# Optimization experiments

Measured on AMD Instinct MI355X. Metric: run time of the kernel, lower is better.

## Reference

```python
import jax, jax.numpy as jnp
import numpy as np

DIM = 96
NH = 8
HID = int(DIM * 2.66)  # 255
B, H, W = 2, 128, 128


def _conv(x, w, groups=1, pad=0):
    # NCHW conv, stride 1
    return jax.lax.conv_general_dilated(
        x, w, (1, 1), ((pad, pad), (pad, pad)),
        feature_group_count=groups,
        dimension_numbers=('NCHW', 'OIHW', 'NCHW'))


def _ln(x, w, b):
    # WithBias LayerNorm over the channel axis (torch does to_3d -> LN(dim) -> to_4d)
    mu = x.mean(axis=1, keepdims=True)
    var = ((x - mu) ** 2).mean(axis=1, keepdims=True)
    return (x - mu) * jax.lax.rsqrt(var + 1e-5) * w[None, :, None, None] + b[None, :, None, None]


def setup_inputs() -> dict:
    key = jax.random.key(0)
    ks = jax.random.split(key, 16)
    d, h2, h4 = DIM, 2 * HID, 4 * HID
    def n(k, shape, s):
        return jax.random.normal(k, shape, jnp.float32) * s
    return {
        'x': jax.random.normal(ks[0], (B, d, H, W), jnp.float32),
        'norm1_w': jnp.ones((d,), jnp.float32), 'norm1_b': jnp.zeros((d,), jnp.float32),
        'qkv_w': n(ks[1], (3 * d, d, 1, 1), 0.05),
        'qkv_dw_w': n(ks[2], (3 * d, 1, 3, 3), 0.1),
        'proj_w': n(ks[3], (d, d, 1, 1), 0.05),
        'temperature': jnp.ones((NH, 1, 1), jnp.float32),
        'thresholdweight': 0.2 * jnp.ones((4, 1, 1, 1), jnp.float32),
        'attn_w1': n(ks[4], (4, NH, NH), 0.2), 'attn_b1': jnp.zeros((4, NH), jnp.float32),
        'attn_w2': n(ks[5], (4, NH, NH), 0.2), 'attn_b2': jnp.zeros((4, NH), jnp.float32),
        'norm2_w': jnp.ones((d,), jnp.float32), 'norm2_b': jnp.zeros((d,), jnp.float32),
        'in_w': n(ks[6], (h2, d, 1, 1), 0.05),
        'main_w': n(ks[7], (h4, 1, 3, 3), 0.1),   # groups=2*HID, 2 out per group
        'lp_w': n(ks[8], (h4, 1, 3, 3), 0.1),     # depthwise
        'hp_w': n(ks[9], (h4, 1, 3, 3), 0.1),     # depthwise
        'ld_w': n(ks[10], (HID, 4, 3, 3), 0.1),   # groups=HID, 4 in per group
        'hd_w': n(ks[11], (HID, 4, 3, 3), 0.1),
        'out_w': n(ks[12], (d, h2, 1, 1), 0.05),
    }


def reference(x, norm1_w, norm1_b, qkv_w, qkv_dw_w, proj_w, temperature,
              thresholdweight, attn_w1, attn_b1, attn_w2, attn_b2,
              norm2_w, norm2_b, in_w, main_w, lp_w, hp_w, ld_w, hd_w, out_w):
    b, c, hh, ww = x.shape
    ch = c // NH
    # ---- STS channel attention ----
    xn = _ln(x, norm1_w, norm1_b)
    qkv = _conv(_conv(xn, qkv_w), qkv_dw_w, groups=3 * c, pad=1)
    q, k, v = jnp.split(qkv, 3, axis=1)
    q = q.reshape(b, NH, ch, hh * ww)
    k = k.reshape(b, NH, ch, hh * ww)
    v = v.reshape(b, NH, ch, hh * ww)
    q = q / jnp.maximum(jnp.linalg.norm(q, axis=-1, keepdims=True), 1e-12)
    k = k / jnp.maximum(jnp.linalg.norm(k, axis=-1, keepdims=True), 1e-12)
    attn = jnp.einsum('bhcn,bhdn->bhcd', q, k) * temperature[None]  # [b,NH,ch,ch]

    def sts_gen(w1, b1, w2, b2):
        a_abs = jnp.abs(attn)
        avg = a_abs.mean(axis=(-2, -1))                       # [b, NH] (GAP)
        g = jax.nn.sigmoid(jnp.maximum(avg @ w1.T + b1, 0.0) @ w2.T + b2)
        thr = (avg * g)[:, :, None, None]
        return jnp.sign(attn) * jnp.maximum(a_abs - thr, 0.0)

    comp = jax.vmap(sts_gen)(attn_w1, attn_b1, attn_w2, attn_b2)  # [4,b,NH,ch,ch]
    comp = jax.nn.softmax(comp, axis=-1)
    attn_c = jnp.sum(comp * thresholdweight.reshape(4, 1, 1, 1, 1), axis=0)
    out = jnp.einsum('bhcd,bhdn->bhcn', attn_c, v).reshape(b, c, hh, ww)
    x = x + _conv(out, proj_w)

    # ---- DeCoupleConvv3 FFN ----
    y = _ln(x, norm2_w, norm2_b)
    y = _conv(y, in_w)                                         # [b, 2*HID, h, w]
    y = jax.nn.relu(_conv(y, main_w, groups=2 * HID, pad=1))   # [b, 4*HID, h, w]
    avg_w = jnp.full((4 * HID, 1, 3, 3), 1.0 / 9.0, y.dtype)   # fixed, non-trainable
    yp = jnp.pad(y, ((0, 0), (0, 0), (1, 1), (1, 1)), mode='edge')  # replicate pad
    l = _conv(yp, avg_w, groups=4 * HID, pad=0)
    hb = y - l
    l = jax.nn.relu(_conv(l, lp_w, groups=4 * HID, pad=1))
    hb = jax.nn.relu(_conv(hb, hp_w, groups=4 * HID, pad=1))
    l_tol, l_toh = jnp.split(l, [2 * HID], axis=1)
    h_toh, h_tol = jnp.split(hb, [2 * HID], axis=1)
    l2 = jax.nn.relu(_conv(jnp.concatenate([l_tol, h_tol], axis=1), ld_w, groups=HID, pad=1))
    h2 = jax.nn.relu(_conv(jnp.concatenate([h_toh, l_toh], axis=1), hd_w, groups=HID, pad=1))
    ffo = _conv(jnp.concatenate([l2, h2], axis=1), out_w)
    return x + ffo
```

## Files before the change

kernel.cpp:

```cpp
#include <hip/hip_runtime.h>
#include <hip/hip_bf16.h>
#include <hip/hip_fp16.h>

#define NB   2
#define NC   96
#define NW   128
#define NPIX 16384
#define NHD  8
#define CHD  12
#define HIDC 255
#define H2C  510
#define H4C  1020

typedef __hip_bfloat16 bf16;
typedef unsigned short u16;
typedef unsigned int   u32;
typedef __half2 h2t;

typedef __attribute__((ext_vector_type(8))) __bf16 bfrag;
typedef __attribute__((ext_vector_type(4))) float  ffrag;

__device__ __forceinline__ float bfu(u16 u)  { return __uint_as_float(((u32)u) << 16); }
__device__ __forceinline__ float bflo(u32 u) { return __uint_as_float(u << 16); }
__device__ __forceinline__ float bfhi(u32 u) { return __uint_as_float(u & 0xffff0000u); }
__device__ __forceinline__ u16 f2u16(float a) {
    bf16 x = __float2bfloat16(a); return *(u16*)&x;
}
__device__ __forceinline__ u32 packbf(float a, float b) {
    return (u32)f2u16(a) | ((u32)f2u16(b) << 16);
}
__device__ __forceinline__ uint4 pack8(const float o[8]) {
    uint4 r; r.x = packbf(o[0], o[1]); r.y = packbf(o[2], o[3]);
    r.z = packbf(o[4], o[5]); r.w = packbf(o[6], o[7]); return r;
}

__device__ __forceinline__ h2t H2u(u32 v) { return __builtin_bit_cast(h2t, v); }
__device__ __forceinline__ u32 U32h(h2t v) { return __builtin_bit_cast(u32, v); }
__device__ __forceinline__ h2t relu2(h2t v) {
    u32 r, u = U32h(v);
    asm("v_pk_max_f16 %0, %1, 0" : "=v"(r) : "v"(u));
    return H2u(r);
}
__device__ __forceinline__ h2t wtap(const h2t* a, int idx) {
    u32 u = U32h(a[idx >> 1]);
    u32 r = (idx & 1) ? ((u & 0xFFFF0000u) | (u >> 16)) : ((u << 16) | (u & 0xFFFFu));
    return H2u(r);
}

struct Trip { h2t L, C, R; };
__device__ __forceinline__ Trip shift3(h2t c2, bool repl, int lane) {
    u32 d = U32h(c2);
    u32 up = (u32)__shfl_up((int)d, 1);
    u32 dn = (u32)__shfl_down((int)d, 1);
    if (lane == 0)  up = repl ? (d << 16) : 0u;
    if (lane == 63) dn = repl ? (d >> 16) : 0u;
    Trip t; t.C = c2;
    t.L = H2u((up >> 16) | (d << 16));
    t.R = H2u((d >> 16) | (dn << 16));
    return t;
}
__device__ __forceinline__ h2t ldrow2(const u16* base, int row, int lane) {
    return ((unsigned)row < 128u) ? *(const h2t*)(base + row * NW + lane * 2) : H2u(0u);
}
#define CONV3(W, c, T, Pa, Pb, Pc)                                             \
    Pc = __hfma2(wtap(W, (c)*9+0), T.L, __hfma2(wtap(W, (c)*9+1), T.C,         \
         __hfma2(wtap(W, (c)*9+2), T.R, Pc)));                                 \
    Pb = __hfma2(wtap(W, (c)*9+3), T.L, __hfma2(wtap(W, (c)*9+4), T.C,         \
         __hfma2(wtap(W, (c)*9+5), T.R, Pb)));                                 \
    Pa = __hfma2(wtap(W, (c)*9+6), T.L, __hfma2(wtap(W, (c)*9+7), T.C,         \
         __hfma2(wtap(W, (c)*9+8), T.R, Pa)));

__global__ __launch_bounds__(64) void ffnstream_kernel(
    const u16* __restrict__ yi, const float* __restrict__ main_w,
    const float* __restrict__ lp_w, const float* __restrict__ hp_w,
    const float* __restrict__ ld_w, const float* __restrict__ hd_w,
    u16* __restrict__ cat) {
    const int lane = threadIdx.x;
    const int g = blockIdx.y;
    const int R0 = blockIdx.x * 32, R1 = R0 + 32;
    const int L0 = max(R0 - 2, 0), L1 = min(R1 + 1, 127);
    const int P0 = max(R0 - 1, 0), P1 = min(R1, 127);
    const u16* yib = yi + (size_t)blockIdx.z * H2C * NPIX;
    u16* catb = cat + (size_t)blockIdx.z * H2C * NPIX;
    const u16* s0p = yib + (size_t)(2 * g) * NPIX;
    const u16* s1p = yib + (size_t)(2 * g + 1) * NPIX;

    h2t wm[18], wl[18], wh[18], wd[18], we[18];
    {
        const float* pm = main_w + 36 * g;
        const float* pl = lp_w + 36 * g;
        const float* ph = hp_w + 36 * g;
        const float* pd = ld_w + 36 * g;
        const float* pe = hd_w + 36 * g;
        #pragma unroll
        for (int k = 0; k < 18; ++k) {
            wm[k] = __halves2half2(__float2half(pm[2*k]), __float2half(pm[2*k+1]));
            wl[k] = __halves2half2(__float2half(pl[2*k]), __float2half(pl[2*k+1]));
            wh[k] = __halves2half2(__float2half(ph[2*k]), __float2half(ph[2*k+1]));
            wd[k] = __halves2half2(__float2half(pd[2*k]), __float2half(pd[2*k+1]));
            we[k] = __halves2half2(__float2half(pe[2*k]), __float2half(pe[2*k+1]));
        }
    }
    const h2t z = H2u(0u);
    const __half k9h = __float2half(1.f / 9.f);
    const h2t k9 = __halves2half2(k9h, k9h);

    h2t ymP0[4], ymP1[4], ymP2[4];
    h2t ymRa[4], ymRb[4], ymRc[4];
    h2t lpP0[4], lpP1[4], lpP2[4];
    h2t hpP0[4], hpP1[4], hpP2[4];
    h2t cd0 = z, cd1 = z, cd2 = z;
    h2t ce0 = z, ce1 = z, ce2 = z;
    #pragma unroll
    for (int c = 0; c < 4; ++c) {
        ymP0[c] = ymP1[c] = ymP2[c] = z;
        ymRa[c] = ymRb[c] = ymRc[c] = z;
        lpP0[c] = lpP1[c] = lpP2[c] = z;
        hpP0[c] = hpP1[c] = hpP2[c] = z;
    }

    const int ys = max(R0 - 3, 0) - 1;
    const int ye = R1 + 3;
    h2t cur0 = ldrow2(s0p, ys, lane),     cur1 = ldrow2(s1p, ys, lane);
    h2t nx10 = ldrow2(s0p, ys + 1, lane), nx11 = ldrow2(s1p, ys + 1, lane);
    #pragma unroll 3
    for (int yy = ys; yy <= ye; ++yy) {
        h2t nx20 = ldrow2(s0p, yy + 2, lane), nx21 = ldrow2(s1p, yy + 2, lane);
        {
            Trip t0 = shift3(cur0, false, lane);
            Trip t1 = shift3(cur1, false, lane);
            CONV3(wm, 0, t0, ymP0[0], ymP1[0], ymP2[0]);
            CONV3(wm, 1, t0, ymP0[1], ymP1[1], ymP2[1]);
            CONV3(wm, 2, t1, ymP0[2], ymP1[2], ymP2[2]);
            CONV3(wm, 3, t1, ymP0[3], ymP1[3], ymP2[3]);
        }
        #pragma unroll
        for (int c = 0; c < 4; ++c) {
            h2t n = relu2(ymP0[c]);
            ymRc[c] = ymRb[c]; ymRb[c] = ymRa[c]; ymRa[c] = n;
            ymP0[c] = ymP1[c]; ymP1[c] = ymP2[c]; ymP2[c] = z;
        }
        int y_l = yy - 2;
        if (y_l >= L0 && y_l <= L1) {
            #pragma unroll
            for (int c = 0; c < 4; ++c) {
                h2t top = (y_l == 0)   ? ymRb[c] : ymRc[c];
                h2t bot = (y_l == 127) ? ymRb[c] : ymRa[c];
                h2t vs = __hadd2(__hadd2(top, ymRb[c]), bot);
                Trip tv = shift3(vs, true, lane);
                h2t l  = __hmul2(__hadd2(__hadd2(tv.L, tv.C), tv.R), k9);
                h2t hb = __hsub2(ymRb[c], l);
                Trip tl = shift3(l, false, lane);
                CONV3(wl, c, tl, lpP0[c], lpP1[c], lpP2[c]);
                Trip th = shift3(hb, false, lane);
                CONV3(wh, c, th, hpP0[c], hpP1[c], hpP2[c]);
            }
        }
        int y_p = yy - 3;
        {
            h2t lpN[4], hpN[4];
            #pragma unroll
            for (int c = 0; c < 4; ++c) {
                lpN[c] = relu2(lpP0[c]); hpN[c] = relu2(hpP0[c]);
                lpP0[c] = lpP1[c]; lpP1[c] = lpP2[c]; lpP2[c] = z;
                hpP0[c] = hpP1[c]; hpP1[c] = hpP2[c]; hpP2[c] = z;
            }
            if (y_p >= P0 && y_p <= P1) {
                #pragma unroll
                for (int c = 0; c < 4; ++c) {
                    bool low = (4 * g + c) < H2C;
                    h2t sld = low ? lpN[c] : hpN[c];
                    h2t shd = low ? hpN[c] : lpN[c];
                    Trip ts = shift3(sld, false, lane);
                    CONV3(wd, c, ts, cd0, cd1, cd2);
                    Trip tu = shift3(shd, false, lane);
                    CONV3(we, c, tu, ce0, ce1, ce2);
                }
            }
        }
        int y_c = yy - 4;
        if (y_c >= R0 && y_c < R1) {
            float a0 = fmaxf(__low2float(cd0), 0.f), a1 = fmaxf(__high2float(cd0), 0.f);
            float b0 = fmaxf(__low2float(ce0), 0.f), b1 = fmaxf(__high2float(ce0), 0.f);
            *(u32*)(catb + (size_t)g * NPIX + y_c * NW + lane * 2) = packbf(a0, a1);
            *(u32*)(catb + (size_t)(HIDC + g) * NPIX + y_c * NW + lane * 2) = packbf(b0, b1);
        }
        cd0 = cd1; cd1 = cd2; cd2 = z;
        ce0 = ce1; ce1 = ce2; ce2 = z;
        cur0 = nx10; cur1 = nx11;
        nx10 = nx20; nx11 = nx21;
    }
}

template <typename TOut, bool RES, int OFMT>
__global__ __launch_bounds__(256) void gemm1x1_kernel(
    const u16* __restrict__ Bm, const float* __restrict__ Am,
    const float* __restrict__ res, TOut* __restrict__ Cm,
    int M, int K, size_t strideB, size_t strideC, size_t strideA) {
    __shared__ u16 Ash[64 * 40];
    __shared__ u16 Bsh[128 * 40];
    const u16* Bz = Bm + (size_t)blockIdx.z * strideB;
    const float* Az = Am + (size_t)blockIdx.z * strideA;
    int n0 = blockIdx.x * 128;
    int m0 = blockIdx.y * 64;
    int tid = threadIdx.x;
    int w = tid >> 6, l15 = tid & 15, q = (tid & 63) >> 4;
    int amm = tid >> 2, akc = (tid & 3) * 8;
    int bkk = tid >> 3, bs0 = tid & 7;

    ffrag acc[8];
    #pragma unroll
    for (int nt = 0; nt < 8; ++nt)
        #pragma unroll
        for (int e = 0; e < 4; ++e) acc[nt][e] = 0.f;

    for (int k0 = 0; k0 < K; k0 += 32) {
        {
            int gm = m0 + amm;
            float f[8];
            #pragma unroll
            for (int e = 0; e < 8; ++e) {
                int gk = k0 + akc + e;
                f[e] = (gm < M && gk < K) ? Az[(size_t)gm * K + gk] : 0.f;
            }
            u32* dst = (u32*)&Ash[amm * 40 + akc];
            #pragma unroll
            for (int e = 0; e < 4; ++e) dst[e] = packbf(f[2 * e], f[2 * e + 1]);
        }
        {
            int gk = k0 + bkk;
            bool ok = gk < K;
            const u16* src = Bz + (size_t)gk * NPIX + n0;
            #pragma unroll
            for (int pass = 0; pass < 2; ++pass) {
                int nn = (bs0 + pass * 8) * 8;
                if (ok) {
                    uint4 v = *(const uint4*)(src + nn);
                    Bsh[(nn + 0) * 40 + bkk] = (u16)(v.x & 0xffff);
                    Bsh[(nn + 1) * 40 + bkk] = (u16)(v.x >> 16);
                    Bsh[(nn + 2) * 40 + bkk] = (u16)(v.y & 0xffff);
                    Bsh[(nn + 3) * 40 + bkk] = (u16)(v.y >> 16);
                    Bsh[(nn + 4) * 40 + bkk] = (u16)(v.z & 0xffff);
                    Bsh[(nn + 5) * 40 + bkk] = (u16)(v.z >> 16);
                    Bsh[(nn + 6) * 40 + bkk] = (u16)(v.w & 0xffff);
                    Bsh[(nn + 7) * 40 + bkk] = (u16)(v.w >> 16);
                } else {
                    #pragma unroll
                    for (int e = 0; e < 8; ++e) Bsh[(nn + e) * 40 + bkk] = 0;
                }
            }
        }
        __syncthreads();
        bfrag af = *(const bfrag*)&Ash[(w * 16 + l15) * 40 + q * 8];
        #pragma unroll
        for (int nt = 0; nt < 8; ++nt) {
            bfrag bf = *(const bfrag*)&Bsh[(nt * 16 + l15) * 40 + q * 8];
            acc[nt] = __builtin_amdgcn_mfma_f32_16x16x32_bf16(af, bf, acc[nt], 0, 0, 0);
        }
        __syncthreads();
    }
    TOut* Cz = Cm + (size_t)blockIdx.z * strideC;
    const float* rz = res + (RES ? (size_t)blockIdx.z * strideC : 0);
    int mrow = m0 + w * 16 + q * 4;
    #pragma unroll
    for (int nt = 0; nt < 8; ++nt) {
        int col = n0 + nt * 16 + l15;
        #pragma unroll
        for (int r = 0; r < 4; ++r) {
            int row = mrow + r;
            if (row < M) {
                float v = acc[nt][r];
                if (RES) v += rz[(size_t)row * NPIX + col];
                if constexpr (OFMT == 0) {
                    ((float*)Cz)[(size_t)row * NPIX + col] = v;
                } else if constexpr (OFMT == 1) {
                    ((u16*)Cz)[(size_t)row * NPIX + col] = f2u16(v);
                } else {
                    __half hh = __float2half(v);
                    ((u16*)Cz)[(size_t)row * NPIX + col] = __builtin_bit_cast(u16, hh);
                }
            }
        }
    }
}

__global__ __launch_bounds__(256) void ln_kernel(
    const float* __restrict__ x, const float* __restrict__ g,
    const float* __restrict__ bta, u16* __restrict__ out) {
    int blk = blockIdx.x;
    int b = blk >> 9;
    int p = ((blk & 511) << 5) + (threadIdx.x & 31);
    int cg = threadIdx.x >> 5;
    const float* xb = x + (size_t)b * NC * NPIX + p;
    float v[12]; float s = 0.f, s2 = 0.f;
    #pragma unroll
    for (int j = 0; j < 12; ++j) {
        float t = xb[(size_t)(cg * 12 + j) * NPIX];
        v[j] = t; s += t; s2 += t * t;
    }
    __shared__ float ss[8][32], qq[8][32], smu[32], sinv[32];
    ss[cg][threadIdx.x & 31] = s; qq[cg][threadIdx.x & 31] = s2;
    __syncthreads();
    if (threadIdx.x < 32) {
        float S = 0.f, Q = 0.f;
        #pragma unroll
        for (int k = 0; k < 8; ++k) { S += ss[k][threadIdx.x]; Q += qq[k][threadIdx.x]; }
        float mu = S * (1.f / NC);
        float var = Q * (1.f / NC) - mu * mu;
        smu[threadIdx.x] = mu; sinv[threadIdx.x] = rsqrtf(var + 1e-5f);
    }
    __syncthreads();
    float mu = smu[threadIdx.x & 31], inv = sinv[threadIdx.x & 31];
    u16* ob = out + (size_t)b * NC * NPIX + p;
    #pragma unroll
    for (int j = 0; j < 12; ++j) {
        int c = cg * 12 + j;
        ob[(size_t)c * NPIX] = f2u16((v[j] - mu) * inv * g[c] + bta[c]);
    }
}

__device__ __forceinline__ void load_row_zpad(const u16* ib, int iy, int x0, float a[10]) {
    if (iy < 0 || iy >= NW) {
        #pragma unroll
        for (int k = 0; k < 10; ++k) a[k] = 0.f;
        return;
    }
    const u16* rp = ib + iy * NW;
    uint4 v = *(const uint4*)(rp + x0);
    a[1]=bflo(v.x); a[2]=bfhi(v.x); a[3]=bflo(v.y); a[4]=bfhi(v.y);
    a[5]=bflo(v.z); a[6]=bfhi(v.z); a[7]=bflo(v.w); a[8]=bfhi(v.w);
    a[0] = (x0 > 0)   ? bfu(rp[x0 - 1]) : 0.f;
    a[9] = (x0 < 120) ? bfu(rp[x0 + 8]) : 0.f;
}

template <bool RELU>
__global__ __launch_bounds__(256) void dwconv3x3_kernel(
    const u16* __restrict__ in, const float* __restrict__ w,
    u16* __restrict__ out, int CHN, int ICN, int idiv) {
    int id = blockIdx.x * 256 + threadIdx.x;
    int ty = id >> 4, tx = id & 15;
    int y0 = ty * 4, x0 = tx * 8;
    int b = blockIdx.y / CHN, oc = blockIdx.y % CHN;
    int ic = oc / idiv;
    const u16* ib = in + ((size_t)b * ICN + ic) * NPIX;
    float a[6][10];
    #pragma unroll
    for (int k = 0; k < 6; ++k) load_row_zpad(ib, y0 - 1 + k, x0, a[k]);
    const float* wr = w + (size_t)oc * 9;
    float w9[9];
    #pragma unroll
    for (int k = 0; k < 9; ++k) w9[k] = wr[k];
    u16* ob = out + ((size_t)b * CHN + oc) * NPIX + y0 * NW + x0;
    #pragma unroll
    for (int jr = 0; jr < 4; ++jr) {
        float o[8];
        #pragma unroll
        for (int j = 0; j < 8; ++j) {
            float s = 0.f;
            #pragma unroll
            for (int r = 0; r < 3; ++r)
                #pragma unroll
                for (int kx = 0; kx < 3; ++kx)
                    s += w9[r * 3 + kx] * a[jr + r][j + kx];
            o[j] = RELU ? fmaxf(s, 0.f) : s;
        }
        *(uint4*)(ob + jr * NW) = pack8(o);
    }
}

__global__ __launch_bounds__(256) void qknorm_kernel(
    const u16* __restrict__ qkv2, float* __restrict__ scales) {
    int r = blockIdx.x;
    int b = r / 192, ch = r % 192;
    const u16* src = qkv2 + ((size_t)b * 288 + ch) * NPIX;
    float s = 0.f;
    for (int p = threadIdx.x * 8; p < NPIX; p += 2048) {
        uint4 v = *(const uint4*)(src + p);
        float f[8];
        f[0]=bflo(v.x); f[1]=bfhi(v.x); f[2]=bflo(v.y); f[3]=bfhi(v.y);
        f[4]=bflo(v.z); f[5]=bfhi(v.z); f[6]=bflo(v.w); f[7]=bfhi(v.w);
        #pragma unroll
        for (int k = 0; k < 8; ++k) s += f[k] * f[k];
    }
    #pragma unroll
    for (int off = 32; off > 0; off >>= 1) s += __shfl_down(s, off, 64);
    __shared__ float part[4];
    int wid = threadIdx.x >> 6;
    if ((threadIdx.x & 63) == 0) part[wid] = s;
    __syncthreads();
    if (threadIdx.x == 0) {
        float tot = part[0] + part[1] + part[2] + part[3];
        scales[r] = 1.f / fmaxf(sqrtf(tot), 1e-12f);
    }
}

__global__ __launch_bounds__(256) void attn_kernel(
    const u16* __restrict__ qkv2, float* __restrict__ attn_raw) {
    int blk = blockIdx.y;
    int slice = blockIdx.x;
    int i = blk % CHD; int h = (blk / CHD) % NHD; int b = blk / (CHD * NHD);
    const u16* q = qkv2 + ((size_t)b * 288 + h * CHD + i) * NPIX;
    const u16* k = qkv2 + ((size_t)b * 288 + 96 + h * CHD) * NPIX;
    float acc[CHD];
    #pragma unroll
    for (int j = 0; j < CHD; ++j) acc[j] = 0.f;
    int p0 = slice * 4096;
    #pragma unroll
    for (int it = 0; it < 2; ++it) {
        int p = p0 + it * 2048 + threadIdx.x * 8;
        uint4 qv = *(const uint4*)(q + p);
        float qf[8];
        qf[0]=bflo(qv.x); qf[1]=bfhi(qv.x); qf[2]=bflo(qv.y); qf[3]=bfhi(qv.y);
        qf[4]=bflo(qv.z); qf[5]=bfhi(qv.z); qf[6]=bflo(qv.w); qf[7]=bfhi(qv.w);
        #pragma unroll
        for (int j = 0; j < CHD; ++j) {
            uint4 kv = *(const uint4*)(k + (size_t)j * NPIX + p);
            float s = qf[0]*bflo(kv.x) + qf[1]*bfhi(kv.x) + qf[2]*bflo(kv.y) + qf[3]*bfhi(kv.y)
                    + qf[4]*bflo(kv.z) + qf[5]*bfhi(kv.z) + qf[6]*bflo(kv.w) + qf[7]*bfhi(kv.w);
            acc[j] += s;
        }
    }
    __shared__ float part[4][CHD];
    int wid = threadIdx.x >> 6, lane = threadIdx.x & 63;
    #pragma unroll
    for (int j = 0; j < CHD; ++j) {
        float v = acc[j];
        #pragma unroll
        for (int off = 32; off > 0; off >>= 1) v += __shfl_down(v, off, 64);
        if (lane == 0) part[wid][j] = v;
    }
    __syncthreads();
    if (threadIdx.x < CHD) {
        int j = threadIdx.x;
        float d = part[0][j] + part[1][j] + part[2][j] + part[3][j];
        atomicAdd(&attn_raw[(size_t)blk * CHD + j], d);
    }
}

__global__ __launch_bounds__(256) void sts_kernel(
    const float* __restrict__ attn, const float* __restrict__ scl,
    const float* __restrict__ temp, const float* __restrict__ tw,
    const float* __restrict__ w1, const float* __restrict__ b1,
    const float* __restrict__ w2, const float* __restrict__ b2,
    const float* __restrict__ proj_w, float* __restrict__ Wm) {
    int b = blockIdx.x;
    __shared__ float sat[NHD * CHD * CHD];
    __shared__ float sac[NHD * CHD * CHD];
    __shared__ float avg[NHD];
    __shared__ float thr[4][NHD];
    for (int idx = threadIdx.x; idx < NHD * CHD * CHD; idx += 256) {
        int h = idx / (CHD * CHD); int r = idx % (CHD * CHD);
        int i = r / CHD, j = r % CHD;
        sat[idx] = attn[(size_t)b * NHD * CHD * CHD + idx]
                 * scl[b * 192 + h * CHD + i] * scl[b * 192 + 96 + h * CHD + j] * temp[h];
    }
    __syncthreads();
    if (threadIdx.x < NHD) {
        float s = 0.f;
        for (int t = 0; t < CHD * CHD; ++t) s += fabsf(sat[threadIdx.x * CHD * CHD + t]);
        avg[threadIdx.x] = s * (1.f / (CHD * CHD));
    }
    __syncthreads();
    if (threadIdx.x < 4) {
        int s = threadIdx.x;
        float t1[NHD];
        for (int hp = 0; hp < NHD; ++hp) {
            float u = b1[s * NHD + hp];
            for (int h = 0; h < NHD; ++h) u += avg[h] * w1[s * 64 + hp * NHD + h];
            t1[hp] = fmaxf(u, 0.f);
        }
        for (int hp = 0; hp < NHD; ++hp) {
            float u = b2[s * NHD + hp];
            for (int h = 0; h < NHD; ++h) u += t1[h] * w2[s * 64 + hp * NHD + h];
            float gg = 1.f / (1.f + expf(-u));
            thr[s][hp] = avg[hp] * gg;
        }
    }
    __syncthreads();
    if (threadIdx.x < NHD * CHD) {
        int h = threadIdx.x / CHD, i = threadIdx.x % CHD;
        const float* arow = sat + (h * CHD + i) * CHD;
        float acc[CHD];
        #pragma unroll
        for (int j = 0; j < CHD; ++j) acc[j] = 0.f;
        for (int s = 0; s < 4; ++s) {
            float comp[CHD]; float m = -1e30f;
            #pragma unroll
            for (int j = 0; j < CHD; ++j) {
                float a = arow[j];
                float sg = (a > 0.f) ? 1.f : ((a < 0.f) ? -1.f : 0.f);
                float c = sg * fmaxf(fabsf(a) - thr[s][h], 0.f);
                comp[j] = c; m = fmaxf(m, c);
            }
            float sum = 0.f;
            #pragma unroll
            for (int j = 0; j < CHD; ++j) { comp[j] = expf(comp[j] - m); sum += comp[j]; }
            float wts2v = tw[s] / sum;
            #pragma unroll
            for (int j = 0; j < CHD; ++j) acc[j] += wts2v * comp[j];
        }
        for (int j = 0; j < CHD; ++j)
            sac[(h * CHD + i) * CHD + j] = acc[j];
    }
    __syncthreads();
    float* Wb = Wm + (size_t)b * NC * NC;
    for (int idx = threadIdx.x; idx < NC * NC; idx += 256) {
        int m = idx / NC, col = idx % NC;
        int h = col / CHD, j = col % CHD;
        const float* pr = proj_w + m * NC + h * CHD;
        const float* ar = sac + h * CHD * CHD + j;
        float s = 0.f;
        #pragma unroll
        for (int i = 0; i < CHD; ++i) s += pr[i] * ar[i * CHD];
        Wb[idx] = s;
    }
}

extern "C" void kernel_launch(void* const* d_in, const int* in_sizes, int n_in,
                              void* d_out, int out_size, void* d_ws, size_t ws_size,
                              hipStream_t stream) {
    const float* x       = (const float*)d_in[0];
    const float* norm1_w = (const float*)d_in[1];
    const float* norm1_b = (const float*)d_in[2];
    const float* qkv_w   = (const float*)d_in[3];
    const float* qkv_dw  = (const float*)d_in[4];
    const float* proj_w  = (const float*)d_in[5];
    const float* temp    = (const float*)d_in[6];
    const float* thw     = (const float*)d_in[7];
    const float* aw1     = (const float*)d_in[8];
    const float* ab1     = (const float*)d_in[9];
    const float* aw2     = (const float*)d_in[10];
    const float* ab2     = (const float*)d_in[11];
    const float* norm2_w = (const float*)d_in[12];
    const float* norm2_b = (const float*)d_in[13];
    const float* in_w    = (const float*)d_in[14];
    const float* main_w  = (const float*)d_in[15];
    const float* lp_w    = (const float*)d_in[16];
    const float* hp_w    = (const float*)d_in[17];
    const float* ld_w    = (const float*)d_in[18];
    const float* hd_w    = (const float*)d_in[19];
    const float* out_w   = (const float*)d_in[20];
    float* out = (float*)d_out;

    char* ws = (char*)d_ws;
    float* x1    = (float*)(ws + 0);
    u16*   xnb   = (u16*)(ws + 12582912);
    u16*   qkv1  = (u16*)(ws + 18874368);
    u16*   qkv2  = (u16*)(ws + 37748736);
    float* scl   = (float*)(ws + 56623104);
    float* attn  = (float*)(ws + 56639488);
    char*  F0    = ws + 56672256;
    float* Wm    = (float*)(ws + 56655872);
    const size_t S_full = 33423360;
    bool full = ws_size >= (size_t)56672256 + S_full;

    dim3 blk(256);
    ln_kernel<<<dim3(NB * NPIX / 32), blk, 0, stream>>>(x, norm1_w, norm1_b, xnb);
    gemm1x1_kernel<u16, false, 1><<<dim3(128, 5, NB), blk, 0, stream>>>(
        xnb, qkv_w, nullptr, qkv1, 288, 96, (size_t)NC * NPIX, (size_t)288 * NPIX, 0);
    dwconv3x3_kernel<false><<<dim3(2, NB * 288), blk, 0, stream>>>(
        qkv1, qkv_dw, qkv2, 288, 288, 1);
    qknorm_kernel<<<dim3(NB * 192), blk, 0, stream>>>(qkv2, scl);
    (void)hipMemsetAsync(attn, 0, (size_t)NB * NHD * CHD * CHD * sizeof(float), stream);
    attn_kernel<<<dim3(4, NB * NHD * CHD), blk, 0, stream>>>(qkv2, attn);
    sts_kernel<<<dim3(NB), blk, 0, stream>>>(attn, scl, temp, thw, aw1, ab1, aw2, ab2,
                                             proj_w, Wm);
    gemm1x1_kernel<float, true, 0><<<dim3(128, 2, NB), blk, 0, stream>>>(
        qkv2 + (size_t)192 * NPIX, Wm, x, x1, 96, 96,
        (size_t)288 * NPIX, (size_t)NC * NPIX, (size_t)NC * NC);
    ln_kernel<<<dim3(NB * NPIX / 32), blk, 0, stream>>>(x1, norm2_w, norm2_b, xnb);
    if (full) {
        u16* yi  = qkv1;
        u16* cat = (u16*)F0;
        gemm1x1_kernel<u16, false, 2><<<dim3(128, 8, NB), blk, 0, stream>>>(
            xnb, in_w, nullptr, yi, H2C, 96, (size_t)NC * NPIX, (size_t)H2C * NPIX, 0);
        ffnstream_kernel<<<dim3(4, HIDC, NB), dim3(64), 0, stream>>>(
            yi, main_w, lp_w, hp_w, ld_w, hd_w, cat);
        gemm1x1_kernel<float, true, 0><<<dim3(128, 2, NB), blk, 0, stream>>>(
            cat, out_w, x1, out, 96, H2C, (size_t)H2C * NPIX, (size_t)NC * NPIX, 0);
    } else {
        for (int b = 0; b < NB; ++b) {
            u16* yi  = qkv1;
            u16* cat = qkv2;
            gemm1x1_kernel<u16, false, 2><<<dim3(128, 8, 1), blk, 0, stream>>>(
                xnb + (size_t)b * NC * NPIX, in_w, nullptr, yi, H2C, 96, 0, 0, 0);
            ffnstream_kernel<<<dim3(4, HIDC, 1), dim3(64), 0, stream>>>(
                yi, main_w, lp_w, hp_w, ld_w, hd_w, cat);
            gemm1x1_kernel<float, true, 0><<<dim3(128, 2, 1), blk, 0, stream>>>(
                cat, out_w, x1 + (size_t)b * NC * NPIX, out + (size_t)b * NC * NPIX,
                96, H2C, 0, 0, 0);
        }
    }
}
```

Measured before the change: 361.1 us.

## Fuse LayerNorm into 1x1 GEMMs and q/k norm into depthwise conv

Removes both standalone LayerNorm kernels. The qkv and FFN-input 1x1 GEMMs now compute per-pixel mean and variance from the fp32 input and normalize while staging the B tile, so the bf16 normalized intermediate is no longer written and read back. The q/k L2-norm pass is folded into the depthwise conv, which accumulates squared sums by atomicAdd into a zero-initialized buffer, and the sts kernel now takes the reciprocal sqrt and splits its abs-sum reduction. The cost is that every m-block of a GEMM recomputes the LN statistics and reads fp32 input instead of bf16, and the atomics make the reduction order non-deterministic.

```diff
diff --git a/kernel.cpp b/kernel.cpp
--- a/kernel.cpp
+++ b/kernel.cpp
@@ -192,15 +192,20 @@
     }
 }
 
-template <typename TOut, bool RES, int OFMT>
+template <typename TOut, bool RES, int OFMT, bool LNF = false>
 __global__ __launch_bounds__(256) void gemm1x1_kernel(
     const u16* __restrict__ Bm, const float* __restrict__ Am,
     const float* __restrict__ res, TOut* __restrict__ Cm,
-    int M, int K, size_t strideB, size_t strideC, size_t strideA) {
+    int M, int K, size_t strideB, size_t strideC, size_t strideA,
+    const float* __restrict__ xf, const float* __restrict__ lng,
+    const float* __restrict__ lnb) {
     __shared__ u16 Ash[64 * 40];
     __shared__ u16 Bsh[128 * 40];
+    __shared__ float lmu[128], linv[128];
+    __shared__ float sred[2][128], qred[2][128];
     const u16* Bz = Bm + (size_t)blockIdx.z * strideB;
     const float* Az = Am + (size_t)blockIdx.z * strideA;
+    const float* xz = LNF ? (xf + (size_t)blockIdx.z * NC * NPIX) : nullptr;
     int n0 = blockIdx.x * 128;
     int m0 = blockIdx.y * 64;
     int tid = threadIdx.x;
@@ -208,6 +213,26 @@
     int amm = tid >> 2, akc = (tid & 3) * 8;
     int bkk = tid >> 3, bs0 = tid & 7;
 
+    if constexpr (LNF) {
+        int p = tid & 127, hh = tid >> 7;
+        float s = 0.f, s2 = 0.f;
+        #pragma unroll
+        for (int c = 0; c < 48; ++c) {
+            float v = xz[(size_t)(hh * 48 + c) * NPIX + n0 + p];
+            s += v; s2 += v * v;
+        }
+        sred[hh][p] = s; qred[hh][p] = s2;
+        __syncthreads();
+        if (tid < 128) {
+            float S = sred[0][tid] + sred[1][tid];
+            float Q = qred[0][tid] + qred[1][tid];
+            float m = S * (1.f / NC);
+            float va = Q * (1.f / NC) - m * m;
+            lmu[tid] = m; linv[tid] = rsqrtf(va + 1e-5f);
+        }
+        __syncthreads();
+    }
+
     ffrag acc[8];
     #pragma unroll
     for (int nt = 0; nt < 8; ++nt)
@@ -227,7 +252,23 @@
             #pragma unroll
             for (int e = 0; e < 4; ++e) dst[e] = packbf(f[2 * e], f[2 * e + 1]);
         }
-        {
+        if constexpr (LNF) {
+            int gk = k0 + bkk;
+            const float* src = xz + (size_t)gk * NPIX + n0;
+            float gc = lng[gk], bc = lnb[gk];
+            #pragma unroll
+            for (int pass = 0; pass < 2; ++pass) {
+                int nn = (bs0 + pass * 8) * 8;
+                float4 f0 = *(const float4*)(src + nn);
+                float4 f1 = *(const float4*)(src + nn + 4);
+                float f[8] = {f0.x, f0.y, f0.z, f0.w, f1.x, f1.y, f1.z, f1.w};
+                #pragma unroll
+                for (int e = 0; e < 8; ++e) {
+                    float nv = (f[e] - lmu[nn + e]) * linv[nn + e] * gc + bc;
+                    Bsh[(nn + e) * 40 + bkk] = f2u16(nv);
+                }
+            }
+        } else {
             int gk = k0 + bkk;
             bool ok = gk < K;
             const u16* src = Bz + (size_t)gk * NPIX + n0;
@@ -284,41 +325,6 @@
     }
 }
 
-__global__ __launch_bounds__(256) void ln_kernel(
-    const float* __restrict__ x, const float* __restrict__ g,
-    const float* __restrict__ bta, u16* __restrict__ out) {
-    int blk = blockIdx.x;
-    int b = blk >> 9;
-    int p = ((blk & 511) << 5) + (threadIdx.x & 31);
-    int cg = threadIdx.x >> 5;
-    const float* xb = x + (size_t)b * NC * NPIX + p;
-    float v[12]; float s = 0.f, s2 = 0.f;
-    #pragma unroll
-    for (int j = 0; j < 12; ++j) {
-        float t = xb[(size_t)(cg * 12 + j) * NPIX];
-        v[j] = t; s += t; s2 += t * t;
-    }
-    __shared__ float ss[8][32], qq[8][32], smu[32], sinv[32];
-    ss[cg][threadIdx.x & 31] = s; qq[cg][threadIdx.x & 31] = s2;
-    __syncthreads();
-    if (threadIdx.x < 32) {
-        float S = 0.f, Q = 0.f;
-        #pragma unroll
-        for (int k = 0; k < 8; ++k) { S += ss[k][threadIdx.x]; Q += qq[k][threadIdx.x]; }
-        float mu = S * (1.f / NC);
-        float var = Q * (1.f / NC) - mu * mu;
-        smu[threadIdx.x] = mu; sinv[threadIdx.x] = rsqrtf(var + 1e-5f);
-    }
-    __syncthreads();
-    float mu = smu[threadIdx.x & 31], inv = sinv[threadIdx.x & 31];
-    u16* ob = out + (size_t)b * NC * NPIX + p;
-    #pragma unroll
-    for (int j = 0; j < 12; ++j) {
-        int c = cg * 12 + j;
-        ob[(size_t)c * NPIX] = f2u16((v[j] - mu) * inv * g[c] + bta[c]);
-    }
-}
-
 __device__ __forceinline__ void load_row_zpad(const u16* ib, int iy, int x0, float a[10]) {
     if (iy < 0 || iy >= NW) {
         #pragma unroll
@@ -336,7 +342,8 @@
 template <bool RELU>
 __global__ __launch_bounds__(256) void dwconv3x3_kernel(
     const u16* __restrict__ in, const float* __restrict__ w,
-    u16* __restrict__ out, int CHN, int ICN, int idiv) {
+    u16* __restrict__ out, int CHN, int ICN, int idiv,
+    float* __restrict__ sqsum) {
     int id = blockIdx.x * 256 + threadIdx.x;
     int ty = id >> 4, tx = id & 15;
     int y0 = ty * 4, x0 = tx * 8;
@@ -351,6 +358,7 @@
     #pragma unroll
     for (int k = 0; k < 9; ++k) w9[k] = wr[k];
     u16* ob = out + ((size_t)b * CHN + oc) * NPIX + y0 * NW + x0;
+    float s2 = 0.f;
     #pragma unroll
     for (int jr = 0; jr < 4; ++jr) {
         float o[8];
@@ -363,34 +371,19 @@
                 for (int kx = 0; kx < 3; ++kx)
                     s += w9[r * 3 + kx] * a[jr + r][j + kx];
             o[j] = RELU ? fmaxf(s, 0.f) : s;
+            s2 += o[j] * o[j];
         }
         *(uint4*)(ob + jr * NW) = pack8(o);
     }
-}
-
-__global__ __launch_bounds__(256) void qknorm_kernel(
-    const u16* __restrict__ qkv2, float* __restrict__ scales) {
-    int r = blockIdx.x;
-    int b = r / 192, ch = r % 192;
-    const u16* src = qkv2 + ((size_t)b * 288 + ch) * NPIX;
-    float s = 0.f;
-    for (int p = threadIdx.x * 8; p < NPIX; p += 2048) {
-        uint4 v = *(const uint4*)(src + p);
-        float f[8];
-        f[0]=bflo(v.x); f[1]=bfhi(v.x); f[2]=bflo(v.y); f[3]=bfhi(v.y);
-        f[4]=bflo(v.z); f[5]=bfhi(v.z); f[6]=bflo(v.w); f[7]=bfhi(v.w);
-        #pragma unroll
-        for (int k = 0; k < 8; ++k) s += f[k] * f[k];
-    }
-    #pragma unroll
-    for (int off = 32; off > 0; off >>= 1) s += __shfl_down(s, off, 64);
-    __shared__ float part[4];
-    int wid = threadIdx.x >> 6;
-    if ((threadIdx.x & 63) == 0) part[wid] = s;
-    __syncthreads();
-    if (threadIdx.x == 0) {
-        float tot = part[0] + part[1] + part[2] + part[3];
-        scales[r] = 1.f / fmaxf(sqrtf(tot), 1e-12f);
+    if (oc < 192) {
+        #pragma unroll
+        for (int off = 32; off > 0; off >>= 1) s2 += __shfl_down(s2, off, 64);
+        __shared__ float prt[4];
+        int wid = threadIdx.x >> 6;
+        if ((threadIdx.x & 63) == 0) prt[wid] = s2;
+        __syncthreads();
+        if (threadIdx.x == 0)
+            atomicAdd(&sqsum[b * 192 + oc], prt[0] + prt[1] + prt[2] + prt[3]);
     }
 }
 
@@ -438,7 +431,7 @@
 }
 
 __global__ __launch_bounds__(256) void sts_kernel(
-    const float* __restrict__ attn, const float* __restrict__ scl,
+    const float* __restrict__ attn, const float* __restrict__ sclr,
     const float* __restrict__ temp, const float* __restrict__ tw,
     const float* __restrict__ w1, const float* __restrict__ b1,
     const float* __restrict__ w2, const float* __restrict__ b2,
@@ -446,18 +439,34 @@
     int b = blockIdx.x;
     __shared__ float sat[NHD * CHD * CHD];
     __shared__ float sac[NHD * CHD * CHD];
+    __shared__ float srs[192];
+    __shared__ float pavg[NHD * CHD];
     __shared__ float avg[NHD];
     __shared__ float thr[4][NHD];
+    if (threadIdx.x < 192) {
+        float r = sclr[b * 192 + threadIdx.x];
+        srs[threadIdx.x] = 1.f / fmaxf(sqrtf(r), 1e-12f);
+    }
+    __syncthreads();
     for (int idx = threadIdx.x; idx < NHD * CHD * CHD; idx += 256) {
         int h = idx / (CHD * CHD); int r = idx % (CHD * CHD);
         int i = r / CHD, j = r % CHD;
         sat[idx] = attn[(size_t)b * NHD * CHD * CHD + idx]
-                 * scl[b * 192 + h * CHD + i] * scl[b * 192 + 96 + h * CHD + j] * temp[h];
+                 * srs[h * CHD + i] * srs[96 + h * CHD + j] * temp[h];
+    }
+    __syncthreads();
+    if (threadIdx.x < NHD * CHD) {
+        float s = 0.f;
+        const float* row = sat + threadIdx.x * CHD;
+        #pragma unroll
+        for (int j = 0; j < CHD; ++j) s += fabsf(row[j]);
+        pavg[threadIdx.x] = s;
     }
     __syncthreads();
     if (threadIdx.x < NHD) {
         float s = 0.f;
-        for (int t = 0; t < CHD * CHD; ++t) s += fabsf(sat[threadIdx.x * CHD * CHD + t]);
+        #pragma unroll
+        for (int i = 0; i < CHD; ++i) s += pavg[threadIdx.x * CHD + i];
         avg[threadIdx.x] = s * (1.f / (CHD * CHD));
     }
     __syncthreads();
@@ -544,51 +553,52 @@
 
     char* ws = (char*)d_ws;
     float* x1    = (float*)(ws + 0);
-    u16*   xnb   = (u16*)(ws + 12582912);
     u16*   qkv1  = (u16*)(ws + 18874368);
     u16*   qkv2  = (u16*)(ws + 37748736);
     float* scl   = (float*)(ws + 56623104);
-    float* attn  = (float*)(ws + 56639488);
+    float* attn  = (float*)(ws + 56624640);
     char*  F0    = ws + 56672256;
     float* Wm    = (float*)(ws + 56655872);
     const size_t S_full = 33423360;
     bool full = ws_size >= (size_t)56672256 + S_full;
 
     dim3 blk(256);
-    ln_kernel<<<dim3(NB * NPIX / 32), blk, 0, stream>>>(x, norm1_w, norm1_b, xnb);
-    gemm1x1_kernel<u16, false, 1><<<dim3(128, 5, NB), blk, 0, stream>>>(
-        xnb, qkv_w, nullptr, qkv1, 288, 96, (size_t)NC * NPIX, (size_t)288 * NPIX, 0);
+    (void)hipMemsetAsync(scl, 0, 10752, stream);
+    gemm1x1_kernel<u16, false, 1, true><<<dim3(128, 5, NB), blk, 0, stream>>>(
+        nullptr, qkv_w, nullptr, qkv1, 288, 96, 0, (size_t)288 * NPIX, 0,
+        x, norm1_w, norm1_b);
     dwconv3x3_kernel<false><<<dim3(2, NB * 288), blk, 0, stream>>>(
-        qkv1, qkv_dw, qkv2, 288, 288, 1);
-    qknorm_kernel<<<dim3(NB * 192), blk, 0, stream>>>(qkv2, scl);
-    (void)hipMemsetAsync(attn, 0, (size_t)NB * NHD * CHD * CHD * sizeof(float), stream);
+        qkv1, qkv_dw, qkv2, 288, 288, 1, scl);
     attn_kernel<<<dim3(4, NB * NHD * CHD), blk, 0, stream>>>(qkv2, attn);
     sts_kernel<<<dim3(NB), blk, 0, stream>>>(attn, scl, temp, thw, aw1, ab1, aw2, ab2,
                                              proj_w, Wm);
     gemm1x1_kernel<float, true, 0><<<dim3(128, 2, NB), blk, 0, stream>>>(
         qkv2 + (size_t)192 * NPIX, Wm, x, x1, 96, 96,
-        (size_t)288 * NPIX, (size_t)NC * NPIX, (size_t)NC * NC);
-    ln_kernel<<<dim3(NB * NPIX / 32), blk, 0, stream>>>(x1, norm2_w, norm2_b, xnb);
+        (size_t)288 * NPIX, (size_t)NC * NPIX, (size_t)NC * NC,
+        nullptr, nullptr, nullptr);
     if (full) {
         u16* yi  = qkv1;
         u16* cat = (u16*)F0;
-        gemm1x1_kernel<u16, false, 2><<<dim3(128, 8, NB), blk, 0, stream>>>(
-            xnb, in_w, nullptr, yi, H2C, 96, (size_t)NC * NPIX, (size_t)H2C * NPIX, 0);
+        gemm1x1_kernel<u16, false, 2, true><<<dim3(128, 8, NB), blk, 0, stream>>>(
+            nullptr, in_w, nullptr, yi, H2C, 96, 0, (size_t)H2C * NPIX, 0,
+            x1, norm2_w, norm2_b);
         ffnstream_kernel<<<dim3(4, HIDC, NB), dim3(64), 0, stream>>>(
             yi, main_w, lp_w, hp_w, ld_w, hd_w, cat);
         gemm1x1_kernel<float, true, 0><<<dim3(128, 2, NB), blk, 0, stream>>>(
-            cat, out_w, x1, out, 96, H2C, (size_t)H2C * NPIX, (size_t)NC * NPIX, 0);
+            cat, out_w, x1, out, 96, H2C, (size_t)H2C * NPIX, (size_t)NC * NPIX, 0,
+            nullptr, nullptr, nullptr);
     } else {
         for (int b = 0; b < NB; ++b) {
             u16* yi  = qkv1;
             u16* cat = qkv2;
-            gemm1x1_kernel<u16, false, 2><<<dim3(128, 8, 1), blk, 0, stream>>>(
-                xnb + (size_t)b * NC * NPIX, in_w, nullptr, yi, H2C, 96, 0, 0, 0);
+            gemm1x1_kernel<u16, false, 2, true><<<dim3(128, 8, 1), blk, 0, stream>>>(
+                nullptr, in_w, nullptr, yi, H2C, 96, 0, 0, 0,
+                x1 + (size_t)b * NC * NPIX, norm2_w, norm2_b);
             ffnstream_kernel<<<dim3(4, HIDC, 1), dim3(64), 0, stream>>>(
                 yi, main_w, lp_w, hp_w, ld_w, hd_w, cat);
             gemm1x1_kernel<float, true, 0><<<dim3(128, 2, 1), blk, 0, stream>>>(
                 cat, out_w, x1 + (size_t)b * NC * NPIX, out + (size_t)b * NC * NPIX,
-                96, H2C, 0, 0, 0);
-        }
-    }
-}
+                96, H2C, 0, 0, 0, nullptr, nullptr, nullptr);
+        }
+    }
+}
```

New measurement: 353.8 us. 2.0% less time.
